# Optimization experiments

Measured on AMD Instinct MI355X. Metric: run time of the kernel, lower is better.

The kernel has to match this reference:

```python
import jax, jax.numpy as jnp
import numpy as np

B, S, T = 32, 2048, 768
NH, DH, DHID = 8, 96, 384  # num_heads, head_dim, hidden_dim=4*head_dim


def setup_inputs() -> dict:
    key = jax.random.key(0)
    k = jax.random.split(key, 7)
    token_embeddings = jax.random.normal(k[0], (B, S, T), dtype=jnp.float32)
    attention_mask = jnp.ones((B, S), dtype=jnp.float32)
    # per-head Linear params, stacked on a leading head axis (PyTorch default-ish init scale)
    P_w = jax.random.normal(k[1], (NH, T, DH), dtype=jnp.float32) * (1.0 / np.sqrt(T))
    P_b = jax.random.normal(k[2], (NH, DH), dtype=jnp.float32) * 0.01
    W1_w = jax.random.normal(k[3], (NH, DH, DHID), dtype=jnp.float32) * (1.0 / np.sqrt(DH))
    W1_b = jax.random.normal(k[4], (NH, DHID), dtype=jnp.float32) * 0.01
    W2_w = jax.random.normal(k[5], (NH, DHID, DH), dtype=jnp.float32) * (1.0 / np.sqrt(DHID))
    W2_b = jax.random.normal(k[6], (NH, DH), dtype=jnp.float32) * 0.01
    return {
        'token_embeddings': token_embeddings,
        'attention_mask': attention_mask,
        'P_w': P_w, 'P_b': P_b,
        'W1_w': W1_w, 'W1_b': W1_b,
        'W2_w': W2_w, 'W2_b': W2_b,
    }


def reference(token_embeddings, attention_mask, P_w, P_b, W1_w, W1_b, W2_w, W2_b):
    # Batched over heads instead of the original Python loop; same math per head.
    # H_i = P_i(H): (B, NH, S, DH)
    Hi = jnp.einsum('bst,htd->bhsd', token_embeddings, P_w) + P_b[None, :, None, :]
    # A_i = W2_i(relu(W1_i(H_i))): (B, NH, S, DH)
    A = jax.nn.relu(jnp.einsum('bhsd,hde->bhse', Hi, W1_w) + W1_b[None, :, None, :])
    A = jnp.einsum('bhse,hed->bhsd', A, W2_w) + W2_b[None, :, None, :]
    # masked softmax over the sequence axis (log(mask) adds -inf at padded tokens)
    log_mask = jnp.log(attention_mask)[:, None, :, None]  # (B,1,S,1)
    A = jax.nn.softmax(A + log_mask, axis=2)
    # weighted sum over tokens: (B, NH, DH)
    v = jnp.sum(Hi * A, axis=2)
    # concat heads -> (B, NH*DH) == (B, sentence_dim)
    return v.reshape(v.shape[0], NH * DH)
```

## Files before the change

kernel.cpp:

```cpp
#include <hip/hip_runtime.h>
#include <cstdint>
#include <cstddef>

#define Bsz   32
#define Ssz   2048
#define Tsz   768
#define NH    8
#define DH    96
#define DHID  384
#define Ncols (NH*DH)

using u16 = unsigned short;
typedef __bf16 bf16x8 __attribute__((ext_vector_type(8)));
typedef __bf16 bf16x4 __attribute__((ext_vector_type(4)));
typedef float  f32x4  __attribute__((ext_vector_type(4)));

__device__ __forceinline__ u16 f2bn(float f) {
  __bf16 h = (__bf16)f;
  return __builtin_bit_cast(u16, h);
}
__device__ __forceinline__ float b2f(u16 u) {
  return __builtin_bit_cast(float, (uint32_t)u << 16);
}

__global__ __launch_bounds__(256) void k_pack(const float* __restrict__ Pw,
    const float* __restrict__ W1w, const float* __restrict__ W2w,
    u16* __restrict__ B1t, u16* __restrict__ W1t, u16* __restrict__ W2t)
{
  int i = blockIdx.x * 256 + threadIdx.x;
  if (i < 589824) {
    int n = i / 768, k = i % 768;
    int h = n / 96, d = n % 96;
    B1t[i] = f2bn(Pw[(size_t)h*73728 + (size_t)k*96 + d]);
  } else if (i < 589824 + 294912) {
    int j = i - 589824;
    int h = j / 36864, r = j % 36864;
    int n = r / 96, k = r % 96;
    W1t[j] = f2bn(W1w[(size_t)h*36864 + (size_t)k*384 + n]);
  } else if (i < 589824 + 2*294912) {
    int q = i - 589824 - 294912;
    int h = q / 36864, r = q % 36864;
    int n = r / 384, k = r % 384;
    W2t[q] = f2bn(W2w[(size_t)h*36864 + (size_t)k*96 + n]);
  }
}

__global__ __launch_bounds__(256) void k_gemm1(const float* __restrict__ emb,
    const u16* __restrict__ B1t, const float* __restrict__ Pb, u16* __restrict__ Hi)
{
  __shared__ u16 As[128][40];
  __shared__ u16 Bs[128][40];
  const int tid  = threadIdx.x;
  const int lane = tid & 63;
  const int wid  = tid >> 6;
  const int wr = wid >> 1, wc = wid & 1;
  const int L = blockIdx.x;
  const int widx = (L & 7) * 384 + (L >> 3);
  const int bm = widx / 6, bn = widx % 6;
  const int l15 = lane & 15, lg = lane >> 4;

  f32x4 acc[4][4] = {};
  for (int kt = 0; kt < Tsz/32; ++kt) {
    const int k0 = kt * 32;
    #pragma unroll
    for (int i = 0; i < 4; ++i) {
      int g = tid + i*256;
      int row = g >> 3, seg = g & 7;
      float4 v = *reinterpret_cast<const float4*>(
          emb + (size_t)(bm*128 + row)*Tsz + k0 + seg*4);
      bf16x4 t;
      t[0] = (__bf16)v.x; t[1] = (__bf16)v.y; t[2] = (__bf16)v.z; t[3] = (__bf16)v.w;
      *reinterpret_cast<uint2*>(&As[row][seg*4]) = __builtin_bit_cast(uint2, t);
    }
    #pragma unroll
    for (int i = 0; i < 2; ++i) {
      int g = tid + i*256;
      int row = g >> 2, seg = g & 3;
      uint4 v = *reinterpret_cast<const uint4*>(
          B1t + (size_t)(bn*128 + row)*Tsz + k0 + seg*8);
      *reinterpret_cast<uint4*>(&Bs[row][seg*8]) = v;
    }
    __syncthreads();
    bf16x8 a[4], b[4];
    #pragma unroll
    for (int r = 0; r < 4; ++r)
      a[r] = *reinterpret_cast<const bf16x8*>(&As[wr*64 + r*16 + l15][lg*8]);
    #pragma unroll
    for (int c = 0; c < 4; ++c)
      b[c] = *reinterpret_cast<const bf16x8*>(&Bs[wc*64 + c*16 + l15][lg*8]);
    #pragma unroll
    for (int r = 0; r < 4; ++r)
      #pragma unroll
      for (int c = 0; c < 4; ++c)
        acc[r][c] = __builtin_amdgcn_mfma_f32_16x16x32_bf16(a[r], b[c], acc[r][c], 0, 0, 0);
    __syncthreads();
  }
  #pragma unroll
  for (int c = 0; c < 4; ++c) {
    int col = bn*128 + wc*64 + c*16 + l15;
    float bias = Pb[col];
    #pragma unroll
    for (int r = 0; r < 4; ++r) {
      int row0 = bm*128 + wr*64 + r*16 + lg*4;
      #pragma unroll
      for (int j = 0; j < 4; ++j)
        Hi[(size_t)(row0 + j)*Ncols + col] = f2bn(acc[r][c][j] + bias);
    }
  }
}

__global__ __launch_bounds__(256, 1) void k_ffn_pool(
    const u16* __restrict__ Hi, const u16* __restrict__ W1t, const u16* __restrict__ W2t,
    const float* __restrict__ b1, const float* __restrict__ b2v, const float* __restrict__ mask,
    float* __restrict__ out)
{
  __shared__ u16 W2s[96][392];
  __shared__ u16 Zb[4][2][16][40];
  __shared__ float mb[4][96], lb[4][96], ab[4][96];

  const int tid = threadIdx.x, lane = tid & 63, w = tid >> 6;
  const int l15 = lane & 15, lg = lane >> 4;
  const int h = blockIdx.x, b = blockIdx.y;

  const u16* W1h = W1t + (size_t)h * DHID * DH;
  const u16* W2h = W2t + (size_t)h * DH * DHID;
  const float* b1h = b1 + h * DHID;

  for (int i = tid; i < 96*48; i += 256) {
    int r = i / 48, g = i % 48;
    uint4 v = *reinterpret_cast<const uint4*>(W2h + (size_t)r*DHID + g*8);
    *reinterpret_cast<uint4*>(&W2s[r][g*8]) = v;
  }
  __syncthreads();

  float b2s[6];
  #pragma unroll
  for (int ct = 0; ct < 6; ++ct) b2s[ct] = b2v[h*DH + ct*16 + l15];

  float Mr[6], Lr[6], Ar[6];
  #pragma unroll
  for (int ct = 0; ct < 6; ++ct) { Mr[ct] = -3.4e38f; Lr[ct] = 0.f; Ar[ct] = 0.f; }

  #pragma unroll 1
  for (int pass = 0; pass < 8; ++pass) {
    const size_t prow = (size_t)b*Ssz + (size_t)w*512 + (size_t)pass*64;

    bf16x8 hifr[4][3];
    #pragma unroll
    for (int s = 0; s < 4; ++s)
      #pragma unroll
      for (int ks = 0; ks < 3; ++ks)
        hifr[s][ks] = *reinterpret_cast<const bf16x8*>(
            Hi + (prow + s*16 + l15)*Ncols + h*DH + ks*32 + lg*8);

    f32x4 lgt[4][6] = {};

    #pragma unroll 2
    for (int c = 0; c < 12; ++c) {
      bf16x8 a1c[2][3];
      #pragma unroll
      for (int t = 0; t < 2; ++t)
        #pragma unroll
        for (int ks = 0; ks < 3; ++ks)
          a1c[t][ks] = *reinterpret_cast<const bf16x8*>(
              W1h + (size_t)(c*32 + t*16 + l15)*DH + ks*32 + lg*8);
      float4 bc0 = *reinterpret_cast<const float4*>(b1h + c*32 + lg*4);
      float4 bc1 = *reinterpret_cast<const float4*>(b1h + c*32 + 16 + lg*4);
      bf16x8 b2fr[6];
      #pragma unroll
      for (int ct = 0; ct < 6; ++ct)
        b2fr[ct] = *reinterpret_cast<const bf16x8*>(&W2s[ct*16 + l15][c*32 + lg*8]);

      #pragma unroll
      for (int bi = 0; bi < 2; ++bi) {
        f32x4 z[2][2];
        #pragma unroll
        for (int sl = 0; sl < 2; ++sl) {
          z[sl][0] = f32x4{}; z[sl][1] = f32x4{};
          #pragma unroll
          for (int ks = 0; ks < 3; ++ks) {
            z[sl][0] = __builtin_amdgcn_mfma_f32_16x16x32_bf16(a1c[0][ks], hifr[bi*2+sl][ks], z[sl][0], 0, 0, 0);
            z[sl][1] = __builtin_amdgcn_mfma_f32_16x16x32_bf16(a1c[1][ks], hifr[bi*2+sl][ks], z[sl][1], 0, 0, 0);
          }
        }
        #pragma unroll
        for (int sl = 0; sl < 2; ++sl) {
          bf16x4 p0, p1;
          p0[0] = (__bf16)fmaxf(z[sl][0][0] + bc0.x, 0.f);
          p0[1] = (__bf16)fmaxf(z[sl][0][1] + bc0.y, 0.f);
          p0[2] = (__bf16)fmaxf(z[sl][0][2] + bc0.z, 0.f);
          p0[3] = (__bf16)fmaxf(z[sl][0][3] + bc0.w, 0.f);
          p1[0] = (__bf16)fmaxf(z[sl][1][0] + bc1.x, 0.f);
          p1[1] = (__bf16)fmaxf(z[sl][1][1] + bc1.y, 0.f);
          p1[2] = (__bf16)fmaxf(z[sl][1][2] + bc1.z, 0.f);
          p1[3] = (__bf16)fmaxf(z[sl][1][3] + bc1.w, 0.f);
          *reinterpret_cast<uint2*>(&Zb[w][sl][l15][lg*4])      = __builtin_bit_cast(uint2, p0);
          *reinterpret_cast<uint2*>(&Zb[w][sl][l15][16 + lg*4]) = __builtin_bit_cast(uint2, p1);
        }
        #pragma unroll
        for (int sl = 0; sl < 2; ++sl) {
          bf16x8 zf = *reinterpret_cast<const bf16x8*>(&Zb[w][sl][l15][lg*8]);
          #pragma unroll
          for (int ct = 0; ct < 6; ++ct)
            lgt[bi*2+sl][ct] = __builtin_amdgcn_mfma_f32_16x16x32_bf16(zf, b2fr[ct], lgt[bi*2+sl][ct], 0, 0, 0);
        }
      }
    }

    float lmv[4][4];
    #pragma unroll
    for (int s = 0; s < 4; ++s) {
      float4 mk = *reinterpret_cast<const float4*>(&mask[prow + s*16 + lg*4]);
      lmv[s][0] = __logf(mk.x); lmv[s][1] = __logf(mk.y);
      lmv[s][2] = __logf(mk.z); lmv[s][3] = __logf(mk.w);
    }
    float G[4][6][4];
    #pragma unroll
    for (int s = 0; s < 4; ++s)
      #pragma unroll
      for (int ct = 0; ct < 6; ++ct)
        #pragma unroll
        for (int j = 0; j < 4; ++j)
          G[s][ct][j] = b2f(Hi[(prow + s*16 + lg*4 + j)*Ncols + h*DH + ct*16 + l15]);

    #pragma unroll
    for (int ct = 0; ct < 6; ++ct) {
      float av[4][4];
      float m16 = -3.4e38f;
      #pragma unroll
      for (int s = 0; s < 4; ++s)
        #pragma unroll
        for (int j = 0; j < 4; ++j) {
          av[s][j] = lgt[s][ct][j] + b2s[ct] + lmv[s][j];
          m16 = fmaxf(m16, av[s][j]);
        }
      m16 = fmaxf(m16, __shfl_xor(m16, 16));
      m16 = fmaxf(m16, __shfl_xor(m16, 32));
      float l16 = 0.f, a16 = 0.f;
      #pragma unroll
      for (int s = 0; s < 4; ++s)
        #pragma unroll
        for (int j = 0; j < 4; ++j) {
          float p = __expf(av[s][j] - m16);
          l16 += p;
          a16 += p * G[s][ct][j];
        }
      l16 += __shfl_xor(l16, 16); l16 += __shfl_xor(l16, 32);
      a16 += __shfl_xor(a16, 16); a16 += __shfl_xor(a16, 32);
      float M2 = fmaxf(Mr[ct], m16);
      float eo = __expf(Mr[ct] - M2), en = __expf(m16 - M2);
      Lr[ct] = Lr[ct]*eo + l16*en;
      Ar[ct] = Ar[ct]*eo + a16*en;
      Mr[ct] = M2;
    }
  }

  if (lane < 16) {
    #pragma unroll
    for (int ct = 0; ct < 6; ++ct) {
      mb[w][ct*16 + l15] = Mr[ct];
      lb[w][ct*16 + l15] = Lr[ct];
      ab[w][ct*16 + l15] = Ar[ct];
    }
  }
  __syncthreads();
  if (tid < 96) {
    float m = fmaxf(fmaxf(mb[0][tid], mb[1][tid]), fmaxf(mb[2][tid], mb[3][tid]));
    float l = 0.f, a = 0.f;
    #pragma unroll
    for (int q = 0; q < 4; ++q) {
      float sc = __expf(mb[q][tid] - m);
      l += lb[q][tid] * sc;
      a += ab[q][tid] * sc;
    }
    out[(size_t)b * Ncols + h*DH + tid] = a / l;
  }
}

extern "C" void kernel_launch(void* const* d_in, const int* in_sizes, int n_in,
                              void* d_out, int out_size, void* d_ws, size_t ws_size,
                              hipStream_t stream)
{
  const float* emb  = (const float*)d_in[0];
  const float* mask = (const float*)d_in[1];
  const float* Pw   = (const float*)d_in[2];
  const float* Pb   = (const float*)d_in[3];
  const float* W1w  = (const float*)d_in[4];
  const float* W1b  = (const float*)d_in[5];
  const float* W2w  = (const float*)d_in[6];
  const float* W2b  = (const float*)d_in[7];
  float* out = (float*)d_out;

  char* ws = (char*)d_ws;
  u16*   Hi  = (u16*)(ws);
  u16*   B1t = (u16*)(ws + 100663296ull);
  u16*   W1t = (u16*)(ws + 101842944ull);
  u16*   W2t = (u16*)(ws + 102432768ull);

  k_pack<<<dim3(4608), dim3(256), 0, stream>>>(Pw, W1w, W2w, B1t, W1t, W2t);
  k_gemm1<<<dim3(3072), dim3(256), 0, stream>>>(emb, B1t, Pb, Hi);
  k_ffn_pool<<<dim3(8, 32), dim3(256), 0, stream>>>(Hi, W1t, W2t, W1b, W2b, mask, out);
}
```

Before: 304.1 us.

## Load GEMM1 tiles directly to LDS with swizzled layout and K=64 steps

Replaces register-staged global loads in the projection GEMM with global_load_lds direct-to-LDS transfers. The fp32 activations are now kept in LDS as fp32 and converted to bf16 only when MFMA fragments are built. XOR-swizzled LDS layouts are added to avoid bank conflicts, and the K-tile grows from 32 to 64, which halves the number of barriers. This removes VGPR staging and conversion from the load path, but it doubles the A-tile LDS footprint and moves the conversion work into the inner loop. Loads are still not double-buffered.

```diff
diff --git a/kernel.cpp b/kernel.cpp
--- a/kernel.cpp
+++ b/kernel.cpp
@@ -21,6 +21,12 @@
 }
 __device__ __forceinline__ float b2f(u16 u) {
   return __builtin_bit_cast(float, (uint32_t)u << 16);
+}
+
+typedef const __attribute__((address_space(1))) void* gas_t;
+typedef __attribute__((address_space(3))) void* las_t;
+__device__ __forceinline__ void gload16(const void* g, void* s) {
+  __builtin_amdgcn_global_load_lds((gas_t)g, (las_t)s, 16, 0, 0);
 }
 
 __global__ __launch_bounds__(256) void k_pack(const float* __restrict__ Pw,
@@ -48,51 +54,69 @@
 __global__ __launch_bounds__(256) void k_gemm1(const float* __restrict__ emb,
     const u16* __restrict__ B1t, const float* __restrict__ Pb, u16* __restrict__ Hi)
 {
-  __shared__ u16 As[128][40];
-  __shared__ u16 Bs[128][40];
+  __shared__ float As[128*64];
+  __shared__ u16   Bs[128*64];
   const int tid  = threadIdx.x;
   const int lane = tid & 63;
-  const int wid  = tid >> 6;
-  const int wr = wid >> 1, wc = wid & 1;
+  const int w    = tid >> 6;
+  const int wr = w >> 1, wc = w & 1;
   const int L = blockIdx.x;
   const int widx = (L & 7) * 384 + (L >> 3);
   const int bm = widx / 6, bn = widx % 6;
   const int l15 = lane & 15, lg = lane >> 4;
 
+  const int arow_in = lane >> 4;
+  const int achunk  = lane & 15;
+  const int brow_in = lane >> 3;
+  const int bchunk  = lane & 7;
+
   f32x4 acc[4][4] = {};
-  for (int kt = 0; kt < Tsz/32; ++kt) {
-    const int k0 = kt * 32;
+
+  for (int kt = 0; kt < 12; ++kt) {
+    const int k0 = kt * 64;
+    #pragma unroll
+    for (int i = 0; i < 8; ++i) {
+      const int row = (w*8 + i)*4 + arow_in;
+      const int lc  = achunk ^ (row & 15);
+      gload16(emb + (size_t)(bm*128 + row)*Tsz + k0 + lc*4,
+              &As[(w*8 + i)*256]);
+    }
     #pragma unroll
     for (int i = 0; i < 4; ++i) {
-      int g = tid + i*256;
-      int row = g >> 3, seg = g & 7;
-      float4 v = *reinterpret_cast<const float4*>(
-          emb + (size_t)(bm*128 + row)*Tsz + k0 + seg*4);
-      bf16x4 t;
-      t[0] = (__bf16)v.x; t[1] = (__bf16)v.y; t[2] = (__bf16)v.z; t[3] = (__bf16)v.w;
-      *reinterpret_cast<uint2*>(&As[row][seg*4]) = __builtin_bit_cast(uint2, t);
-    }
-    #pragma unroll
-    for (int i = 0; i < 2; ++i) {
-      int g = tid + i*256;
-      int row = g >> 2, seg = g & 3;
-      uint4 v = *reinterpret_cast<const uint4*>(
-          B1t + (size_t)(bn*128 + row)*Tsz + k0 + seg*8);
-      *reinterpret_cast<uint4*>(&Bs[row][seg*8]) = v;
+      const int row = (w*4 + i)*8 + brow_in;
+      const int lc  = bchunk ^ brow_in;
+      gload16(B1t + (size_t)(bn*128 + row)*Tsz + k0 + lc*8,
+              &Bs[(w*4 + i)*512]);
     }
     __syncthreads();
-    bf16x8 a[4], b[4];
-    #pragma unroll
-    for (int r = 0; r < 4; ++r)
-      a[r] = *reinterpret_cast<const bf16x8*>(&As[wr*64 + r*16 + l15][lg*8]);
-    #pragma unroll
-    for (int c = 0; c < 4; ++c)
-      b[c] = *reinterpret_cast<const bf16x8*>(&Bs[wc*64 + c*16 + l15][lg*8]);
-    #pragma unroll
-    for (int r = 0; r < 4; ++r)
-      #pragma unroll
-      for (int c = 0; c < 4; ++c)
-        acc[r][c] = __builtin_amdgcn_mfma_f32_16x16x32_bf16(a[r], b[c], acc[r][c], 0, 0, 0);
+
+    bf16x8 b[4][2];
+    #pragma unroll
+    for (int c = 0; c < 4; ++c) {
+      const int Rb = wc*64 + c*16 + l15;
+      #pragma unroll
+      for (int kk = 0; kk < 2; ++kk)
+        b[c][kk] = *reinterpret_cast<const bf16x8*>(
+            &Bs[Rb*64 + (((kk*4 + lg) ^ (l15 & 7))*8)]);
+    }
+    #pragma unroll
+    for (int r = 0; r < 4; ++r) {
+      const int R = wr*64 + r*16 + l15;
+      #pragma unroll
+      for (int kk = 0; kk < 2; ++kk) {
+        const int c0 = kk*8 + lg*2;
+        f32x4 fa0 = *reinterpret_cast<const f32x4*>(&As[R*64 + ((c0    ) ^ l15)*4]);
+        f32x4 fa1 = *reinterpret_cast<const f32x4*>(&As[R*64 + ((c0 + 1) ^ l15)*4]);
+        bf16x8 af;
+        af[0] = (__bf16)fa0[0]; af[1] = (__bf16)fa0[1];
+        af[2] = (__bf16)fa0[2]; af[3] = (__bf16)fa0[3];
+        af[4] = (__bf16)fa1[0]; af[5] = (__bf16)fa1[1];
+        af[6] = (__bf16)fa1[2]; af[7] = (__bf16)fa1[3];
+        #pragma unroll
+        for (int c = 0; c < 4; ++c)
+          acc[r][c] = __builtin_amdgcn_mfma_f32_16x16x32_bf16(af, b[c][kk], acc[r][c], 0, 0, 0);
+      }
+    }
     __syncthreads();
   }
   #pragma unroll
```

Result: faster. 284.1 us (-6.6%).
